# Performance work log

Hardware: AMD Instinct MI355X
Metric: run time of the kernel (lower is better)

Reference implementation:

```python
import math
import jax, jax.numpy as jnp
import numpy as np

DIM = 512; DEPTH = 12; HEADS = 8; DIM_HEAD = 64
INNER = HEADS * DIM_HEAD
FF_INNER = 4 * DIM
B = 8192
NUM_TIMESTEPS = 1000
SCALE = 16.0  # cosine_sim_scale
ROT_DIM = 32  # RotaryEmbedding(dim=min(32, dim_head))
NUM_BUCKETS = 32; MAX_DISTANCE = 128


def layer_norm(x, g, eps=1e-5):
    mean = jnp.mean(x, axis=-1, keepdims=True)
    var = jnp.mean((x - mean) ** 2, axis=-1, keepdims=True)  # unbiased=False
    return (x - mean) * jax.lax.rsqrt(var + eps) * g


def l2norm(t):
    n = jnp.linalg.norm(t, axis=-1, keepdims=True)
    return t / jnp.maximum(n, 1e-12)


def rotary_freqs(n):
    inv = 1.0 / (10000.0 ** (jnp.arange(0, ROT_DIM, 2, dtype=jnp.float32) / ROT_DIM))
    f = jnp.arange(n, dtype=jnp.float32)[:, None] * inv[None, :]  # (n, ROT_DIM//2)
    return jnp.repeat(f, 2, axis=-1)  # (n, ROT_DIM), interleaved pairs


def rotate_half(x):
    x1 = x[..., 0::2]; x2 = x[..., 1::2]
    return jnp.stack((-x2, x1), axis=-1).reshape(x.shape)


def apply_rotary(t, freqs):
    tr, tp = t[..., :ROT_DIM], t[..., ROT_DIM:]
    tr = tr * jnp.cos(freqs) + rotate_half(tr) * jnp.sin(freqs)
    return jnp.concatenate([tr, tp], axis=-1)


def rel_pos_bias(i, j, emb):
    rel = jnp.arange(j)[None, :] - jnp.arange(i)[:, None]
    n = jnp.maximum(-rel, 0)
    max_exact = NUM_BUCKETS // 2
    nf = jnp.maximum(n, 1).astype(jnp.float32)
    val_large = max_exact + (jnp.log(nf / max_exact) / math.log(MAX_DISTANCE / max_exact) * (NUM_BUCKETS - max_exact)).astype(jnp.int32)
    val_large = jnp.minimum(val_large, NUM_BUCKETS - 1)
    bucket = jnp.where(n < max_exact, n, val_large)
    return emb[bucket].transpose(2, 0, 1)  # (h, i, j)


def setup_inputs() -> dict:
    key = jax.random.key(0)
    ks = jax.random.split(key, 13)
    w = 0.02
    return {
        "image_embed": jax.random.normal(ks[0], (B, DIM), jnp.float32),
        "text_embed": jax.random.normal(ks[1], (B, DIM), jnp.float32),
        "timesteps": jax.random.randint(ks[2], (B,), 0, NUM_TIMESTEPS),
        "time_emb_table": jax.random.normal(ks[3], (NUM_TIMESTEPS, DIM)) * w,
        "learned_query": jax.random.normal(ks[4], (DIM,)),
        "rel_emb": jax.random.normal(ks[5], (NUM_BUCKETS, HEADS)) * w,
        "attn_norm_g": jnp.ones((DEPTH, DIM)),
        "Wq": jax.random.normal(ks[6], (DEPTH, DIM, INNER)) * w,
        "Wkv": jax.random.normal(ks[7], (DEPTH, DIM, 2 * DIM_HEAD)) * w,
        "null_kv": jax.random.normal(ks[8], (DEPTH, 2, DIM_HEAD)),
        "Wo": jax.random.normal(ks[9], (DEPTH, INNER, DIM)) * w,
        "attn_out_norm_g": jnp.ones((DEPTH, DIM)),
        "ff_norm_g": jnp.ones((DEPTH, DIM)),
        "Wff1": jax.random.normal(ks[10], (DEPTH, DIM, 2 * FF_INNER)) * w,
        "Wff2": jax.random.normal(ks[11], (DEPTH, FF_INNER, DIM)) * w,
        "final_norm_g": jnp.ones((DIM,)),
        "Wproj": jax.random.normal(ks[12], (DIM, DIM)) * w,
    }


def reference(image_embed, text_embed, timesteps, time_emb_table, learned_query, rel_emb,
              attn_norm_g, Wq, Wkv, null_kv, Wo, attn_out_norm_g,
              ff_norm_g, Wff1, Wff2, final_norm_g, Wproj):
    b = image_embed.shape[0]
    # token sequence: [text_embed, time_embed, image_embed, learned_query] -> (b, 4, dim)
    tokens = jnp.concatenate([
        text_embed[:, None, :],
        time_emb_table[timesteps][:, None, :],
        image_embed[:, None, :],
        jnp.broadcast_to(learned_query, (b, 1, DIM)),
    ], axis=1)
    n = tokens.shape[1]
    bias = rel_pos_bias(n, n + 1, rel_emb)            # (h, n, n+1)
    freqs = rotary_freqs(n)                           # (n, ROT_DIM)
    causal = jnp.triu(jnp.ones((n, n + 1), dtype=bool), k=2)
    neg = -jnp.finfo(jnp.float32).max
    sqrt_scale = math.sqrt(SCALE)

    x = tokens
    for l in range(DEPTH):
        # --- Attention ---
        h = layer_norm(x, attn_norm_g[l])
        q = (h @ Wq[l]).reshape(b, n, HEADS, DIM_HEAD).transpose(0, 2, 1, 3) * SCALE
        kv = h @ Wkv[l]
        k, v = kv[..., :DIM_HEAD], kv[..., DIM_HEAD:]  # single-head kv (b, n, d)
        q = apply_rotary(q, freqs)
        k = apply_rotary(k, freqs)
        nk = jnp.broadcast_to(null_kv[l, 0], (b, 1, DIM_HEAD))
        nv = jnp.broadcast_to(null_kv[l, 1], (b, 1, DIM_HEAD))
        k = jnp.concatenate([nk, k], axis=1)
        v = jnp.concatenate([nv, v], axis=1)
        q = l2norm(q) * sqrt_scale
        k = l2norm(k) * sqrt_scale
        sim = jnp.einsum('bhid,bjd->bhij', q, k) + bias[None]
        sim = jnp.where(causal[None, None], neg, sim)
        attn = jax.nn.softmax(sim.astype(jnp.float32), axis=-1).astype(sim.dtype)
        out = jnp.einsum('bhij,bjd->bhid', attn, v).transpose(0, 2, 1, 3).reshape(b, n, INNER)
        x = x + layer_norm(out @ Wo[l], attn_out_norm_g[l])
        # --- SwiGLU FFN ---
        h = layer_norm(x, ff_norm_g[l])
        hg = h @ Wff1[l]
        a, g = hg[..., :FF_INNER], hg[..., FF_INNER:]
        x = x + (a * jax.nn.silu(g)) @ Wff2[l]

    x = layer_norm(x, final_norm_g) @ Wproj
    return x[:, -1, :]  # predicted image embed from learned query position
```

## Files before the change

### kernel.cpp

```cpp
#include <hip/hip_runtime.h>

typedef __bf16 bf16x8 __attribute__((ext_vector_type(8)));
typedef __bf16 bf16x4 __attribute__((ext_vector_type(4)));
typedef __bf16 bf16x2 __attribute__((ext_vector_type(2)));
typedef float  f32x4  __attribute__((ext_vector_type(4)));
typedef unsigned short u16;

#define BATCH   8192
#define NTOK    4
#define ROWS    (BATCH*NTOK)
#define DIM     512
#define HEADS   8
#define DH      64
#define FFI     2048
#define DEPTH   12
#define LN_EPS  1e-5f

static const size_t OFF_WQKV = 0;
static const size_t SZ_WQKV  = 12ull*640*512*2;
static const size_t OFF_WTO  = OFF_WQKV + SZ_WQKV;
static const size_t SZ_WTO   = 12ull*512*512*2;
static const size_t OFF_WTF1 = OFF_WTO + SZ_WTO;
static const size_t SZ_WTF1  = 12ull*4096*512*2;
static const size_t OFF_WTF2 = OFF_WTF1 + SZ_WTF1;
static const size_t SZ_WTF2  = 12ull*512*2048*2;
static const size_t OFF_WTP  = OFF_WTF2 + SZ_WTF2;
static const size_t SZ_WTP   = 512ull*512*2;
static const size_t OFF_X    = OFF_WTP + SZ_WTP;
static const size_t OFF_H    = OFF_X    + (size_t)ROWS*DIM*4;
static const size_t OFF_QKV  = OFF_H    + (size_t)ROWS*DIM*2;
static const size_t OFF_AO   = OFF_QKV  + (size_t)ROWS*640*2;
static const size_t OFF_FLAG = OFF_AO   + (size_t)ROWS*DIM*2;
static const size_t WS_NEED  = OFF_FLAG + 256;

__device__ __forceinline__ float ldf(const void* p, size_t i, bool b16) {
  return b16 ? (float)((const __bf16*)p)[i] : ((const float*)p)[i];
}

__device__ __forceinline__ void gld_lds16(const void* g, void* l) {
  __builtin_amdgcn_global_load_lds((const __attribute__((address_space(1))) void*)g,
                                   (__attribute__((address_space(3))) void*)l, 16, 0, 0);
}

__device__ __forceinline__ float gsum16(float v) {
  #pragma unroll
  for (int o = 8; o > 0; o >>= 1) v += __shfl_xor(v, o, 64);
  return v;
}

__device__ __forceinline__ void wred2(float& a, float& b) {
  #pragma unroll
  for (int o = 32; o > 0; o >>= 1) { a += __shfl_xor(a, o, 64); b += __shfl_xor(b, o, 64); }
}

__global__ void detect_dtype(const unsigned int* __restrict__ w, int* __restrict__ flag) {
  __shared__ int cnt[4];
  int t = threadIdx.x;
  int c = 0;
  for (int i = t; i < 2048; i += 256) {
    unsigned int v = w[i];
    unsigned int lo = v & 0xFFFFu, hi = v >> 16;
    int elo = (int)((lo >> 7) & 0xFF), ehi = (int)((hi >> 7) & 0xFF);
    bool okl = (lo == 0u) || (elo >= 100 && elo <= 140);
    bool okh = (hi == 0u) || (ehi >= 100 && ehi <= 140);
    if (okl && okh) c++;
  }
  #pragma unroll
  for (int o = 32; o > 0; o >>= 1) c += __shfl_down(c, o, 64);
  if ((t & 63) == 0) cnt[t >> 6] = c;
  __syncthreads();
  if (t == 0) flag[0] = (cnt[0] + cnt[1] + cnt[2] + cnt[3] > 1024) ? 1 : 0;
}

__global__ void transpose_any(const void* __restrict__ in, u16* __restrict__ out,
                              int K, int N, size_t out_zsz, int rowoff, int mode,
                              const int* __restrict__ flag) {
  bool b16 = flag[0] != 0;
  __shared__ u16 tile[32][33];
  size_t iboff = (size_t)blockIdx.z * K * N;
  size_t oboff = (size_t)blockIdx.z * out_zsz;
  int n0 = blockIdx.x * 32, k0 = blockIdx.y * 32;
  int tx = threadIdx.x, ty = threadIdx.y;
  #pragma unroll
  for (int r = 0; r < 4; r++) {
    float v = ldf(in, iboff + (size_t)(k0 + ty*4 + r) * N + n0 + tx, b16);
    __bf16 bv = (__bf16)v;
    tile[ty*4+r][tx] = __builtin_bit_cast(u16, bv);
  }
  __syncthreads();
  int rbase;
  if (mode == 0) rbase = rowoff + n0;
  else {
    int s = (n0 >= 2048) ? 1 : 0;
    int np = n0 - s*2048;
    rbase = (np >> 7)*256 + ((np >> 5) & 3)*64 + s*32;
  }
  #pragma unroll
  for (int r = 0; r < 4; r++)
    out[oboff + (size_t)(rbase + ty*4 + r) * K + k0 + tx] = tile[tx][ty*4+r];
}

__global__ void build_tokens(const void* __restrict__ text, const void* __restrict__ img,
                             const int* __restrict__ ts, const void* __restrict__ table,
                             const void* __restrict__ lq, float* __restrict__ x,
                             const int* __restrict__ flag) {
  bool b16 = flag[0] != 0;
  int b = blockIdx.x, t = threadIdx.x;
  float* xr = x + (size_t)b * NTOK * DIM;
  int tsb = ts[b];
  for (int e = t; e < DIM; e += 256) {
    xr[e]         = ldf(text,  (size_t)b * DIM + e, b16);
    xr[DIM + e]   = ldf(table, (size_t)tsb * DIM + e, b16);
    xr[2*DIM + e] = ldf(img,   (size_t)b * DIM + e, b16);
    xr[3*DIM + e] = ldf(lq,    (size_t)e, b16);
  }
}

__global__ void ln_f32_bf16(const float* __restrict__ x, const void* __restrict__ g, size_t goff,
                            __bf16* __restrict__ out, const int* __restrict__ flag) {
  bool b16 = flag[0] != 0;
  int lane = threadIdx.x & 63;
  int row = blockIdx.x * 4 + (threadIdx.x >> 6);
  const float4* xr = (const float4*)(x + (size_t)row * DIM);
  float4 A4 = xr[lane*2], B4 = xr[lane*2 + 1];
  float v[8] = {A4.x, A4.y, A4.z, A4.w, B4.x, B4.y, B4.z, B4.w};
  float s = 0.f, s2 = 0.f;
  #pragma unroll
  for (int e = 0; e < 8; e++) { s += v[e]; s2 += v[e]*v[e]; }
  wred2(s, s2);
  float mean = s * (1.f/DIM);
  float var  = s2 * (1.f/DIM) - mean*mean;
  float rs = rsqrtf(var + LN_EPS);
  bf16x8 ov;
  #pragma unroll
  for (int e = 0; e < 8; e++)
    ov[e] = (__bf16)((v[e]-mean) * rs * ldf(g, goff + lane*8 + e, b16));
  *(bf16x8*)(out + (size_t)row * DIM + lane*8) = ov;
}

__global__ void ln_add_ln(const __bf16* __restrict__ y,
                          const void* __restrict__ g1, size_t g1off,
                          const void* __restrict__ g2, size_t g2off,
                          float* __restrict__ x, __bf16* __restrict__ h,
                          const int* __restrict__ flag) {
  bool b16 = flag[0] != 0;
  int lane = threadIdx.x & 63;
  int row = blockIdx.x * 4 + (threadIdx.x >> 6);
  bf16x8 y8 = *(const bf16x8*)(y + (size_t)row * DIM + lane*8);
  float yv[8];
  float s = 0.f, s2 = 0.f;
  #pragma unroll
  for (int e = 0; e < 8; e++) { yv[e] = (float)y8[e]; s += yv[e]; s2 += yv[e]*yv[e]; }
  wred2(s, s2);
  float mean = s * (1.f/DIM);
  float var  = s2 * (1.f/DIM) - mean*mean;
  float rs = rsqrtf(var + LN_EPS);
  float4* xr = (float4*)(x + (size_t)row * DIM);
  float4 XA = xr[lane*2], XB = xr[lane*2 + 1];
  float xv[8] = {XA.x, XA.y, XA.z, XA.w, XB.x, XB.y, XB.z, XB.w};
  #pragma unroll
  for (int e = 0; e < 8; e++)
    xv[e] += (yv[e]-mean) * rs * ldf(g1, g1off + lane*8 + e, b16);
  xr[lane*2]     = make_float4(xv[0], xv[1], xv[2], xv[3]);
  xr[lane*2 + 1] = make_float4(xv[4], xv[5], xv[6], xv[7]);
  float t = 0.f, t2 = 0.f;
  #pragma unroll
  for (int e = 0; e < 8; e++) { t += xv[e]; t2 += xv[e]*xv[e]; }
  wred2(t, t2);
  float mean2 = t * (1.f/DIM);
  float var2  = t2 * (1.f/DIM) - mean2*mean2;
  float rs2 = rsqrtf(var2 + LN_EPS);
  bf16x8 hv;
  #pragma unroll
  for (int e = 0; e < 8; e++)
    hv[e] = (__bf16)((xv[e]-mean2) * rs2 * ldf(g2, g2off + lane*8 + e, b16));
  *(bf16x8*)(h + (size_t)row * DIM + lane*8) = hv;
}

__global__ void ln_final(const float* __restrict__ x, const void* __restrict__ g,
                         __bf16* __restrict__ out, const int* __restrict__ flag) {
  bool b16 = flag[0] != 0;
  int lane = threadIdx.x & 63;
  int b = blockIdx.x * 4 + (threadIdx.x >> 6);
  int row = b*NTOK + 3;
  const float4* xr = (const float4*)(x + (size_t)row * DIM);
  float4 A4 = xr[lane*2], B4 = xr[lane*2 + 1];
  float v[8] = {A4.x, A4.y, A4.z, A4.w, B4.x, B4.y, B4.z, B4.w};
  float s = 0.f, s2 = 0.f;
  #pragma unroll
  for (int e = 0; e < 8; e++) { s += v[e]; s2 += v[e]*v[e]; }
  wred2(s, s2);
  float mean = s * (1.f/DIM);
  float var  = s2 * (1.f/DIM) - mean*mean;
  float rs = rsqrtf(var + LN_EPS);
  bf16x8 ov;
  #pragma unroll
  for (int e = 0; e < 8; e++)
    ov[e] = (__bf16)((v[e]-mean) * rs * ldf(g, (size_t)lane*8 + e, b16));
  *(bf16x8*)(out + (size_t)b * DIM + lane*8) = ov;
}

template<int BROWS, int EPI>
__global__ __launch_bounds__(512, 2) void gemm8(
    const __bf16* __restrict__ A, int lda,
    const __bf16* __restrict__ B, int ldb,
    void* __restrict__ Cv, int ldc, int K, const int* __restrict__ flag)
{
  constexpr int UNITS = (BROWS == 256) ? 4 : 3;
  constexpr int WCN   = (BROWS == 256) ? 4 : 2;
  constexpr int M_FR  = (BROWS == 256) ? 8 : 4;
  constexpr int QM    = M_FR / 4;
  __shared__ char ldsmem[2][(256 + BROWS) * 128];

  const int tid = threadIdx.x;
  const int wid = tid >> 6, lane = tid & 63;
  const int wr = wid / WCN, wc = wid % WCN;
  const int lr = lane & 15, lc = lane >> 4;
  const int sr = tid >> 3;
  const int cs = ((tid & 7) ^ (sr & 7)) * 8;
  const int bx = blockIdx.x, by = blockIdx.y;

  const __bf16* Ab = A + (size_t)by * 256 * lda;
  const __bf16* Bb = B + (size_t)bx * BROWS * ldb;

  f32x4 acc[M_FR][4] = {};
  const int NT = K >> 6;

  char* lds0 = ldsmem[0];
  char* lds1 = ldsmem[1];

  auto stage_unit = [&](int p, int kt, int u) {
    char* base = (p ? lds1 : lds0);
    if (u < 2) {
      const __bf16* s = Ab + (size_t)(u*128 + sr) * lda + kt*64 + cs;
      char* d = base + u*16384 + (wid << 10);
      gld_lds16(s, d);
      gld_lds16(s + (size_t)64 * lda, d + 8192);
    } else {
      const __bf16* s = Bb + (size_t)((u-2)*128 + sr) * ldb + kt*64 + cs;
      char* d = base + 32768 + (u-2)*16384 + (wid << 10);
      gld_lds16(s, d);
      gld_lds16(s + (size_t)64 * ldb, d + 8192);
    }
  };

  #pragma unroll
  for (int u = 0; u < UNITS; u++) stage_unit(0, 0, u);

  const int NIT = NT >> 1;
  for (int i = 0; i < NIT; i++) {
    const int t1 = 2*i + 1;
    const int t2 = (2*i + 2 < NT) ? (2*i + 2) : 0;
    #pragma unroll
    for (int hfl = 0; hfl < 2; hfl++) {
      char* cbase = hfl ? lds1 : lds0;
      const int sp = hfl ^ 1;
      const int st = hfl ? t2 : t1;
      bf16x8 bfr[4][2];
      #pragma unroll
      for (int q = 0; q < 4; q++) {
        if (q < UNITS) stage_unit(sp, st, q);
        if (q == 0) {
          asm volatile("s_waitcnt vmcnt(2)" ::: "memory");
          asm volatile("s_barrier" ::: "memory");
          #pragma unroll
          for (int f = 0; f < 4; f++)
            #pragma unroll
            for (int kk = 0; kk < 2; kk++) {
              int row = wc*64 + f*16 + lr;
              int ch = (kk*4 + lc) ^ (lr & 7);
              bfr[f][kk] = *(const bf16x8*)(cbase + 32768 + row*128 + ch*16);
            }
        }
        bf16x8 afr[QM][2];
        #pragma unroll
        for (int m2 = 0; m2 < QM; m2++)
          #pragma unroll
          for (int kk = 0; kk < 2; kk++) {
            int row = wr*(M_FR*16) + (q*QM + m2)*16 + lr;
            int ch = (kk*4 + lc) ^ (lr & 7);
            afr[m2][kk] = *(const bf16x8*)(cbase + row*128 + ch*16);
          }
        __builtin_amdgcn_s_setprio(1);
        #pragma unroll
        for (int m2 = 0; m2 < QM; m2++)
          #pragma unroll
          for (int n = 0; n < 4; n++)
            #pragma unroll
            for (int kk = 0; kk < 2; kk++)
              acc[q*QM + m2][n] = __builtin_amdgcn_mfma_f32_16x16x32_bf16(
                  afr[m2][kk], bfr[n][kk], acc[q*QM + m2][n], 0, 0, 0);
        __builtin_amdgcn_s_setprio(0);
        asm volatile("s_barrier" ::: "memory");
      }
    }
  }
  asm volatile("s_waitcnt vmcnt(0)" ::: "memory");

  if (EPI == 1) {
    __bf16* Ob = (__bf16*)Cv;
    const int colb = bx*128 + wc*32 + lr;
    const int rowb = by*256 + wr*128 + lc*4;
    #pragma unroll
    for (int m = 0; m < M_FR; m++)
      #pragma unroll
      for (int rr = 0; rr < 4; rr++) {
        size_t ro = (size_t)(rowb + m*16 + rr) * ldc;
        #pragma unroll
        for (int fa = 0; fa < 2; fa++) {
          float a = acc[m][fa][rr], g = acc[m][fa+2][rr];
          Ob[ro + colb + fa*16] = (__bf16)(a * g / (1.f + __expf(-g)));
        }
      }
  } else {
    __bf16* Cb = (__bf16*)Cv;
    const int colb = bx*BROWS + wc*64 + lr;
    const int rowb = by*256 + wr*(M_FR*16) + lc*4;
    #pragma unroll
    for (int m = 0; m < M_FR; m++)
      #pragma unroll
      for (int rr = 0; rr < 4; rr++) {
        size_t ro = (size_t)(rowb + m*16 + rr) * ldc;
        #pragma unroll
        for (int n = 0; n < 4; n++) Cb[ro + colb + n*16] = (__bf16)acc[m][n][rr];
      }
  }
}

template<int EPI>
__global__ __launch_bounds__(256, 2) void gemm128(
    const __bf16* __restrict__ A, int lda,
    const __bf16* __restrict__ B, int ldb,
    void* __restrict__ Cv, int ldc, int K, const int* __restrict__ flag)
{
  __shared__ char ldsmem[2][32768];
  const int tid = threadIdx.x;
  const int wid = tid >> 6, lane = tid & 63;
  const int wr = wid >> 1, wc = wid & 1;
  const int lr = lane & 15, lc = lane >> 4;
  const int bx = blockIdx.x, by = blockIdx.y;
  const __bf16* Ab = A + (size_t)by * 128 * lda;
  const __bf16* Bb = B + (size_t)bx * 128 * ldb;
  f32x4 acc[4][4] = {};
  const int NT = K >> 6;

  const int rg0 = (wid << 3) + (lane >> 3);
  const int scol = ((lane & 7) ^ (rg0 & 7)) * 8;

  auto stage = [&](char* base, int kt) {
    #pragma unroll
    for (int r = 0; r < 4; r++) {
      gld_lds16(Ab + (size_t)(r*32 + rg0)*lda + kt*64 + scol, base + r*4096 + (wid << 10));
      gld_lds16(Bb + (size_t)(r*32 + rg0)*ldb + kt*64 + scol, base + 16384 + r*4096 + (wid << 10));
    }
  };

  stage(ldsmem[0], 0);
  for (int t = 0; t < NT; t++) {
    char* cbase = ldsmem[t & 1];
    char* sbase = ldsmem[(t & 1) ^ 1];
    stage(sbase, (t + 1 < NT) ? (t + 1) : 0);
    asm volatile("s_waitcnt vmcnt(8)" ::: "memory");
    asm volatile("s_barrier" ::: "memory");
    bf16x8 bfr[4][2];
    #pragma unroll
    for (int f = 0; f < 4; f++)
      #pragma unroll
      for (int kk = 0; kk < 2; kk++) {
        int row = wc*64 + f*16 + lr;
        int ch = (kk*4 + lc) ^ (lr & 7);
        bfr[f][kk] = *(const bf16x8*)(cbase + 16384 + row*128 + ch*16);
      }
    __builtin_amdgcn_s_setprio(1);
    #pragma unroll
    for (int m = 0; m < 4; m++) {
      bf16x8 afr[2];
      #pragma unroll
      for (int kk = 0; kk < 2; kk++) {
        int row = wr*64 + m*16 + lr;
        int ch = (kk*4 + lc) ^ (lr & 7);
        afr[kk] = *(const bf16x8*)(cbase + row*128 + ch*16);
      }
      #pragma unroll
      for (int n = 0; n < 4; n++)
        #pragma unroll
        for (int kk = 0; kk < 2; kk++)
          acc[m][n] = __builtin_amdgcn_mfma_f32_16x16x32_bf16(
              afr[kk], bfr[n][kk], acc[m][n], 0, 0, 0);
    }
    __builtin_amdgcn_s_setprio(0);
    asm volatile("s_barrier" ::: "memory");
  }
  asm volatile("s_waitcnt vmcnt(0)" ::: "memory");

  const int colb = bx*128 + wc*64 + lr;
  const int rowb = by*128 + wr*64 + lc*4;
  if (EPI == 2) {
    float* Xf = (float*)Cv;
    #pragma unroll
    for (int m = 0; m < 4; m++)
      #pragma unroll
      for (int rr = 0; rr < 4; rr++) {
        size_t ro = (size_t)(rowb + m*16 + rr) * ldc;
        #pragma unroll
        for (int n = 0; n < 4; n++) Xf[ro + colb + n*16] += acc[m][n][rr];
      }
  } else if (EPI == 0) {
    __bf16* Cb = (__bf16*)Cv;
    #pragma unroll
    for (int m = 0; m < 4; m++)
      #pragma unroll
      for (int rr = 0; rr < 4; rr++) {
        size_t ro = (size_t)(rowb + m*16 + rr) * ldc;
        #pragma unroll
        for (int n = 0; n < 4; n++) Cb[ro + colb + n*16] = (__bf16)acc[m][n][rr];
      }
  } else {
    bool b16o = flag[0] != 0;
    __bf16* Cb = (__bf16*)Cv;
    float*  Cf = (float*)Cv;
    #pragma unroll
    for (int m = 0; m < 4; m++)
      #pragma unroll
      for (int rr = 0; rr < 4; rr++) {
        size_t ro = (size_t)(rowb + m*16 + rr) * ldc;
        #pragma unroll
        for (int n = 0; n < 4; n++) {
          float val = acc[m][n][rr];
          if (b16o) Cb[ro + colb + n*16] = (__bf16)val; else Cf[ro + colb + n*16] = val;
        }
      }
  }
}

__global__ __launch_bounds__(256) void attn_kernel(
    const __bf16* __restrict__ qkv,
    const void* __restrict__ nkv_all, int layer, const void* __restrict__ rel_emb,
    __bf16* __restrict__ ao, const int* __restrict__ flag)
{
  bool b16 = flag[0] != 0;
  const int tid = threadIdx.x;
  const int w = tid >> 6, l = tid & 63;
  const int g = l >> 4, c = l & 15;
  const int bh = blockIdx.x * 16 + w * 4 + g;
  const int b = bh >> 3, h = bh & 7;
  const bool rot = (c < 8);

  const float LN1E4_32 = 9.210340371976184f * (1.f/32.f);
  float inv0 = __expf(-(float)(4*c)     * LN1E4_32);
  float inv1 = __expf(-(float)(4*c + 2) * LN1E4_32);
  float cs0[4], sn0[4], cs1[4], sn1[4];
  #pragma unroll
  for (int t = 0; t < 4; t++) {
    __sincosf((float)t * inv0, &sn0[t], &cs0[t]);
    __sincosf((float)t * inv1, &sn1[t], &cs1[t]);
  }
  float rb[4];
  #pragma unroll
  for (int t = 0; t < 4; t++) rb[t] = ldf(rel_emb, (size_t)t * 8 + h, b16);

  float q[4][4];
  #pragma unroll
  for (int i = 0; i < 4; i++) {
    bf16x4 qv = *(const bf16x4*)(qkv + ((size_t)(b*NTOK + i)) * 640 + h*DH + c*4);
    float v0 = (float)qv[0], v1 = (float)qv[1], v2 = (float)qv[2], v3 = (float)qv[3];
    if (rot) {
      float n0 = v0*cs0[i] - v1*sn0[i], n1 = v1*cs0[i] + v0*sn0[i];
      float n2 = v2*cs1[i] - v3*sn1[i], n3 = v3*cs1[i] + v2*sn1[i];
      v0 = n0; v1 = n1; v2 = n2; v3 = n3;
    }
    q[i][0] = v0; q[i][1] = v1; q[i][2] = v2; q[i][3] = v3;
  }
  #pragma unroll
  for (int i = 0; i < 4; i++) {
    float ss = q[i][0]*q[i][0] + q[i][1]*q[i][1] + q[i][2]*q[i][2] + q[i][3]*q[i][3];
    float r = 1.f / fmaxf(sqrtf(gsum16(ss)), 1e-12f);
    #pragma unroll
    for (int e = 0; e < 4; e++) q[i][e] *= r;
  }

  float kk[5][4], vv[5][4];
  #pragma unroll
  for (int e = 0; e < 4; e++) {
    kk[0][e] = ldf(nkv_all, (size_t)layer*128 + c*4 + e, b16);
    vv[0][e] = ldf(nkv_all, (size_t)layer*128 + 64 + c*4 + e, b16);
  }
  #pragma unroll
  for (int j = 1; j < 5; j++) {
    const __bf16* base = qkv + ((size_t)(b*NTOK + j - 1)) * 640 + 512;
    bf16x4 kv4 = *(const bf16x4*)(base + c*4);
    bf16x4 vv4 = *(const bf16x4*)(base + 64 + c*4);
    float v0 = (float)kv4[0], v1 = (float)kv4[1], v2 = (float)kv4[2], v3 = (float)kv4[3];
    if (rot) {
      int t = j - 1;
      float n0 = v0*cs0[t] - v1*sn0[t], n1 = v1*cs0[t] + v0*sn0[t];
      float n2 = v2*cs1[t] - v3*sn1[t], n3 = v3*cs1[t] + v2*sn1[t];
      v0 = n0; v1 = n1; v2 = n2; v3 = n3;
    }
    kk[j][0] = v0; kk[j][1] = v1; kk[j][2] = v2; kk[j][3] = v3;
    #pragma unroll
    for (int e = 0; e < 4; e++) vv[j][e] = (float)vv4[e];
  }
  #pragma unroll
  for (int j = 0; j < 5; j++) {
    float ss = kk[j][0]*kk[j][0] + kk[j][1]*kk[j][1] + kk[j][2]*kk[j][2] + kk[j][3]*kk[j][3];
    float r = 1.f / fmaxf(sqrtf(gsum16(ss)), 1e-12f);
    #pragma unroll
    for (int e = 0; e < 4; e++) kk[j][e] *= r;
  }

  #pragma unroll
  for (int i = 0; i < 4; i++) {
    float sim[5];
    #pragma unroll
    for (int j = 0; j < 5; j++) {
      if (j > i + 1) break;
      float pp = q[i][0]*kk[j][0] + q[i][1]*kk[j][1] + q[i][2]*kk[j][2] + q[i][3]*kk[j][3];
      sim[j] = 16.f * gsum16(pp) + rb[(i - j > 0) ? (i - j) : 0];
    }
    float m = sim[0];
    #pragma unroll
    for (int j = 1; j < 5; j++) { if (j > i + 1) break; m = fmaxf(m, sim[j]); }
    float Z = 0.f, o0 = 0.f, o1 = 0.f, o2 = 0.f, o3 = 0.f;
    #pragma unroll
    for (int j = 0; j < 5; j++) {
      if (j > i + 1) break;
      float e = __expf(sim[j] - m);
      Z += e;
      o0 += e * vv[j][0]; o1 += e * vv[j][1]; o2 += e * vv[j][2]; o3 += e * vv[j][3];
    }
    float rz = 1.f / Z;
    bf16x4 ov = { (__bf16)(o0*rz), (__bf16)(o1*rz), (__bf16)(o2*rz), (__bf16)(o3*rz) };
    *(bf16x4*)(ao + ((size_t)(b*NTOK + i)) * DIM + h*DH + c*4) = ov;
  }
}

extern "C" void kernel_launch(void* const* d_in, const int* in_sizes, int n_in,
                              void* d_out, int out_size, void* d_ws, size_t ws_size,
                              hipStream_t stream) {
  const void* image_embed     = d_in[0];
  const void* text_embed      = d_in[1];
  const int*  timesteps       = (const int*)d_in[2];
  const void* time_table      = d_in[3];
  const void* learned_query   = d_in[4];
  const void* rel_emb         = d_in[5];
  const void* attn_norm_g     = d_in[6];
  const void* Wq              = d_in[7];
  const void* Wkv             = d_in[8];
  const void* null_kv         = d_in[9];
  const void* Wo              = d_in[10];
  const void* attn_out_norm_g = d_in[11];
  const void* ff_norm_g       = d_in[12];
  const void* Wff1            = d_in[13];
  const void* Wff2            = d_in[14];
  const void* final_norm_g    = d_in[15];
  const void* Wproj           = d_in[16];

  if (ws_size < WS_NEED) return;

  char* ws = (char*)d_ws;
  __bf16* wqkv = (__bf16*)(ws + OFF_WQKV);
  __bf16* wto  = (__bf16*)(ws + OFF_WTO);
  __bf16* wtf1 = (__bf16*)(ws + OFF_WTF1);
  __bf16* wtf2 = (__bf16*)(ws + OFF_WTF2);
  __bf16* wtp  = (__bf16*)(ws + OFF_WTP);
  float*  x    = (float*) (ws + OFF_X);
  __bf16* h    = (__bf16*)(ws + OFF_H);
  __bf16* qkv  = (__bf16*)(ws + OFF_QKV);
  __bf16* ao   = (__bf16*)(ws + OFF_AO);
  __bf16* act  = (__bf16*)(ws + OFF_QKV);
  int*    flag = (int*)   (ws + OFF_FLAG);

  detect_dtype<<<1, 256, 0, stream>>>((const unsigned int*)Wq, flag);

  dim3 tb(32, 8);
  transpose_any<<<dim3(16, 16, 12),  tb, 0, stream>>>(Wq,   (u16*)wqkv, 512,  512,  640ull*512, 0,   0, flag);
  transpose_any<<<dim3(4,  16, 12),  tb, 0, stream>>>(Wkv,  (u16*)wqkv, 512,  128,  640ull*512, 512, 0, flag);
  transpose_any<<<dim3(16, 16, 12),  tb, 0, stream>>>(Wo,   (u16*)wto,  512,  512,  512ull*512, 0,   0, flag);
  transpose_any<<<dim3(128,16, 12),  tb, 0, stream>>>(Wff1, (u16*)wtf1, 512,  4096, 4096ull*512,0,   1, flag);
  transpose_any<<<dim3(16, 64, 12),  tb, 0, stream>>>(Wff2, (u16*)wtf2, 2048, 512,  512ull*2048,0,   0, flag);
  transpose_any<<<dim3(16, 16, 1),   tb, 0, stream>>>(Wproj,(u16*)wtp,  512,  512,  512ull*512, 0,   0, flag);

  build_tokens<<<BATCH, 256, 0, stream>>>(text_embed, image_embed, timesteps, time_table,
                                          learned_query, x, flag);

  for (int l = 0; l < DEPTH; l++) {
    const __bf16* wqkv_l = wqkv + (size_t)l * 640 * 512;
    const __bf16* wto_l  = wto  + (size_t)l * 512 * 512;
    const __bf16* wtf1_l = wtf1 + (size_t)l * 4096 * 512;
    const __bf16* wtf2_l = wtf2 + (size_t)l * 512 * 2048;

    ln_f32_bf16<<<ROWS/4, 256, 0, stream>>>(x, attn_norm_g, (size_t)l*DIM, h, flag);
    gemm128<0><<<dim3(5, 256), 256, 0, stream>>>(h, DIM, wqkv_l, 512, qkv, 640, 512, flag);
    attn_kernel<<<BATCH/2, 256, 0, stream>>>(qkv, null_kv, l, rel_emb, ao, flag);
    gemm128<0><<<dim3(4, 256), 256, 0, stream>>>(ao, DIM, wto_l, 512, qkv , DIM, 512, flag);
    ln_add_ln<<<ROWS/4, 256, 0, stream>>>(qkv , attn_out_norm_g, (size_t)l*DIM,
                                          ff_norm_g, (size_t)l*DIM, x, h, flag);

    for (int c = 0; c < 2; c++) {
      const __bf16* hc = h + (size_t)c * 16384 * DIM;
      float*        xc = x + (size_t)c * 16384 * DIM;
      gemm8<256,1><<<dim3(16, 64), 512, 0, stream>>>(hc, DIM, wtf1_l, 512, act, FFI, 512, flag);
      gemm128<2><<<dim3(4, 128), 256, 0, stream>>>(act, FFI, wtf2_l, FFI, xc, DIM, 2048, flag);
    }
  }

  ln_final<<<BATCH/4, 256, 0, stream>>>(x, final_norm_g, ao , flag);
  gemm128<3><<<dim3(4, 64), 256, 0, stream>>>(ao, DIM, wtp, 512, d_out, DIM, 512, flag);
}
```

Measured before the change: 5.661 ms.

## Interleave LDS prefetch stages with per-row-block MFMA phases in 128x128 GEMM

```diff
diff --git a/kernel.cpp b/kernel.cpp
--- a/kernel.cpp
+++ b/kernel.cpp
@@ -328,7 +328,7 @@
 }
 
 template<int EPI>
-__global__ __launch_bounds__(256, 2) void gemm128(
+__global__ __launch_bounds__(256, 2) void gemm4(
     const __bf16* __restrict__ A, int lda,
     const __bf16* __restrict__ B, int ldb,
     void* __restrict__ Cv, int ldc, int K, const int* __restrict__ flag)
@@ -343,53 +343,60 @@
   const __bf16* Bb = B + (size_t)bx * 128 * ldb;
   f32x4 acc[4][4] = {};
   const int NT = K >> 6;
-
-  const int rg0 = (wid << 3) + (lane >> 3);
-  const int scol = ((lane & 7) ^ (rg0 & 7)) * 8;
-
-  auto stage = [&](char* base, int kt) {
-    #pragma unroll
-    for (int r = 0; r < 4; r++) {
-      gld_lds16(Ab + (size_t)(r*32 + rg0)*lda + kt*64 + scol, base + r*4096 + (wid << 10));
-      gld_lds16(Bb + (size_t)(r*32 + rg0)*ldb + kt*64 + scol, base + 16384 + r*4096 + (wid << 10));
-    }
+  const int srow = lane >> 3;
+  const int scs  = ((lane & 7) ^ srow) * 8;
+
+  auto stage_unit = [&](int p, int kt, int u) {
+    const bool isA = (u < 2);
+    const int half = u & 1;
+    const int r0 = half*64 + wid*8 + srow;
+    const __bf16* S = isA ? (Ab + (size_t)r0 * lda + kt*64 + scs)
+                          : (Bb + (size_t)r0 * ldb + kt*64 + scs);
+    char* d = ldsmem[p] + (isA ? 0 : 16384) + half*8192 + (wid << 10);
+    gld_lds16(S, d);
+    gld_lds16(S + (size_t)32 * (isA ? lda : ldb), d + 4096);
   };
 
-  stage(ldsmem[0], 0);
+  #pragma unroll
+  for (int u = 0; u < 4; u++) stage_unit(0, 0, u);
+
   for (int t = 0; t < NT; t++) {
-    char* cbase = ldsmem[t & 1];
-    char* sbase = ldsmem[(t & 1) ^ 1];
-    stage(sbase, (t + 1 < NT) ? (t + 1) : 0);
-    asm volatile("s_waitcnt vmcnt(8)" ::: "memory");
-    asm volatile("s_barrier" ::: "memory");
+    const int cp = t & 1, sp = cp ^ 1;
+    char* cbase = ldsmem[cp];
+    const int st = (t + 1 < NT) ? (t + 1) : 0;
     bf16x8 bfr[4][2];
     #pragma unroll
-    for (int f = 0; f < 4; f++)
+    for (int q = 0; q < 4; q++) {
+      stage_unit(sp, st, q);
+      if (q == 0) {
+        asm volatile("s_waitcnt vmcnt(2)" ::: "memory");
+        asm volatile("s_barrier" ::: "memory");
+        #pragma unroll
+        for (int f = 0; f < 4; f++)
+          #pragma unroll
+          for (int kk = 0; kk < 2; kk++) {
+            int row = wc*64 + f*16 + lr;
+            int ch = (kk*4 + lc) ^ (lr & 7);
+            bfr[f][kk] = *(const bf16x8*)(cbase + 16384 + row*128 + ch*16);
+          }
+      }
+      bf16x8 afr[2];
       #pragma unroll
       for (int kk = 0; kk < 2; kk++) {
-        int row = wc*64 + f*16 + lr;
-        int ch = (kk*4 + lc) ^ (lr & 7);
-        bfr[f][kk] = *(const bf16x8*)(cbase + 16384 + row*128 + ch*16);
-      }
-    __builtin_amdgcn_s_setprio(1);
-    #pragma unroll
-    for (int m = 0; m < 4; m++) {
-      bf16x8 afr[2];
-      #pragma unroll
-      for (int kk = 0; kk < 2; kk++) {
-        int row = wr*64 + m*16 + lr;
+        int row = wr*64 + q*16 + lr;
         int ch = (kk*4 + lc) ^ (lr & 7);
         afr[kk] = *(const bf16x8*)(cbase + row*128 + ch*16);
       }
+      __builtin_amdgcn_s_setprio(1);
       #pragma unroll
       for (int n = 0; n < 4; n++)
         #pragma unroll
         for (int kk = 0; kk < 2; kk++)
-          acc[m][n] = __builtin_amdgcn_mfma_f32_16x16x32_bf16(
-              afr[kk], bfr[n][kk], acc[m][n], 0, 0, 0);
-    }
-    __builtin_amdgcn_s_setprio(0);
-    asm volatile("s_barrier" ::: "memory");
+          acc[q][n] = __builtin_amdgcn_mfma_f32_16x16x32_bf16(
+              afr[kk], bfr[n][kk], acc[q][n], 0, 0, 0);
+      __builtin_amdgcn_s_setprio(0);
+      asm volatile("s_barrier" ::: "memory");
+    }
   }
   asm volatile("s_waitcnt vmcnt(0)" ::: "memory");
 
@@ -591,9 +598,9 @@
     const __bf16* wtf2_l = wtf2 + (size_t)l * 512 * 2048;
 
     ln_f32_bf16<<<ROWS/4, 256, 0, stream>>>(x, attn_norm_g, (size_t)l*DIM, h, flag);
-    gemm128<0><<<dim3(5, 256), 256, 0, stream>>>(h, DIM, wqkv_l, 512, qkv, 640, 512, flag);
+    gemm4<0><<<dim3(5, 256), 256, 0, stream>>>(h, DIM, wqkv_l, 512, qkv, 640, 512, flag);
     attn_kernel<<<BATCH/2, 256, 0, stream>>>(qkv, null_kv, l, rel_emb, ao, flag);
-    gemm128<0><<<dim3(4, 256), 256, 0, stream>>>(ao, DIM, wto_l, 512, qkv , DIM, 512, flag);
+    gemm4<0><<<dim3(4, 256), 256, 0, stream>>>(ao, DIM, wto_l, 512, qkv , DIM, 512, flag);
     ln_add_ln<<<ROWS/4, 256, 0, stream>>>(qkv , attn_out_norm_g, (size_t)l*DIM,
                                           ff_norm_g, (size_t)l*DIM, x, h, flag);
 
@@ -601,10 +608,10 @@
       const __bf16* hc = h + (size_t)c * 16384 * DIM;
       float*        xc = x + (size_t)c * 16384 * DIM;
       gemm8<256,1><<<dim3(16, 64), 512, 0, stream>>>(hc, DIM, wtf1_l, 512, act, FFI, 512, flag);
-      gemm128<2><<<dim3(4, 128), 256, 0, stream>>>(act, FFI, wtf2_l, FFI, xc, DIM, 2048, flag);
+      gemm4<2><<<dim3(4, 128), 256, 0, stream>>>(act, FFI, wtf2_l, FFI, xc, DIM, 2048, flag);
     }
   }
 
   ln_final<<<BATCH/4, 256, 0, stream>>>(x, final_norm_g, ao , flag);
-  gemm128<3><<<dim3(4, 64), 256, 0, stream>>>(ao, DIM, wtp, 512, d_out, DIM, 512, flag);
-}
+  gemm4<3><<<dim3(4, 64), 256, 0, stream>>>(ao, DIM, wtp, 512, d_out, DIM, 512, flag);
+}
```

After: 5.713 ms. About the same (+0.9%).
